# Kernel optimization log

Hardware: AMD Instinct MI355X
Metric: run time of the kernel (lower is better)

Reference implementation:

```python
import jax, jax.numpy as jnp
from jax import lax
import numpy as np

IN_DIM = 5
HID = 512
SEQ = 250
BATCH = 256


def setup_inputs() -> dict:
    key = jax.random.key(0)
    ks = jax.random.split(key, 7)
    s = 1.0 / np.sqrt(HID)  # PyTorch LSTMCell init scale
    strokes = jax.random.normal(ks[0], (BATCH, SEQ, IN_DIM), dtype=jnp.float32)
    W_ih = jax.random.uniform(ks[1], (4 * HID, IN_DIM), minval=-s, maxval=s, dtype=jnp.float32)
    W_hh = jax.random.uniform(ks[2], (4 * HID, HID), minval=-s, maxval=s, dtype=jnp.float32)
    b_ih = jax.random.uniform(ks[3], (4 * HID,), minval=-s, maxval=s, dtype=jnp.float32)
    b_hh = jax.random.uniform(ks[4], (4 * HID,), minval=-s, maxval=s, dtype=jnp.float32)
    W_out = jax.random.uniform(ks[5], (1, HID), minval=-s, maxval=s, dtype=jnp.float32)
    b_out = jax.random.uniform(ks[6], (1,), minval=-s, maxval=s, dtype=jnp.float32)
    return {"strokes": strokes, "W_ih": W_ih, "W_hh": W_hh, "b_ih": b_ih,
            "b_hh": b_hh, "W_out": W_out, "b_out": b_out}


def reference(strokes, W_ih, W_hh, b_ih, b_hh, W_out, b_out):
    B = strokes.shape[0]
    # Precompute input projections for all timesteps (one big GEMM instead of SEQ small ones)
    # x_proj: [T, B, 4H]
    x_proj = jnp.einsum('bti,gi->tbg', strokes, W_ih) + b_ih + b_hh
    h0 = jnp.zeros((B, HID), dtype=strokes.dtype)
    c0 = jnp.zeros((B, HID), dtype=strokes.dtype)

    def step(carry, xp):
        h, c = carry
        gates = xp + h @ W_hh.T  # [B, 4H]; PyTorch gate order: i, f, g, o
        i, f, g, o = jnp.split(gates, 4, axis=-1)
        c = jax.nn.sigmoid(f) * c + jax.nn.sigmoid(i) * jnp.tanh(g)
        h = jax.nn.sigmoid(o) * jnp.tanh(c)
        return (h, c), None

    (h, _), _ = lax.scan(step, (h0, c0), x_proj)
    raw = (h @ W_out.T + b_out).squeeze(-1)  # [B]
    return jax.nn.sigmoid(jax.nn.leaky_relu(raw, 0.1))
```

## Files before the change

kernel.cpp:

```cpp
#include <hip/hip_runtime.h>
#include <hip/hip_bf16.h>

#define BATCH 256
#define SEQ   250
#define HID   512
#define INDIM 5

#define NBLK  256
#define NCH   16
#define MB    16
#define HB    32
#define NMEM  16

#define LROWU 36
#define LMEMU 576
#define SLOT_BYTES (BATCH * HID * 2)

typedef __attribute__((ext_vector_type(8))) short short8;
typedef __attribute__((ext_vector_type(4))) float f32x4;
typedef __attribute__((ext_vector_type(4))) unsigned int u32x4;

__device__ __forceinline__ float sigmoidf_fast(float x) {
  return 1.0f / (1.0f + __expf(-x));
}
__device__ __forceinline__ float tanhf_fast(float x) {
  return 2.0f / (1.0f + __expf(-2.0f * x)) - 1.0f;
}
__device__ __forceinline__ unsigned short f2bf_rne(float x) {
  union { float f; unsigned u; } v; v.f = x;
  unsigned r = v.u + 0x7fffu + ((v.u >> 16) & 1u);
  return (unsigned short)(r >> 16);
}
__device__ __forceinline__ float bf2f(unsigned short h) {
  union { unsigned u; float f; } v; v.u = ((unsigned)h) << 16;
  return v.f;
}

__global__ __launch_bounds__(256, 1) void lstm_persist(
    const float* __restrict__ strokes, const float* __restrict__ W_ih,
    const float* __restrict__ W_hh, const float* __restrict__ b_ih,
    const float* __restrict__ b_hh, const float* __restrict__ W_out,
    const float* __restrict__ b_out, float* __restrict__ out,
    unsigned short* __restrict__ hbuf,
    int* __restrict__ flagsML,
    int* __restrict__ flagsL2,
    int* __restrict__ xcd_ids,
    int* __restrict__ vflag)
{
  const int tid  = threadIdx.x;
  const int bid  = blockIdx.x;
  const int bt   = bid & 15;
  const int ht   = bid >> 4;
  const int wv   = tid >> 6;
  const int lane = tid & 63;
  const int n16  = lane & 15;
  const int q    = lane >> 4;

  __shared__ unsigned short h_lds[NMEM * LMEMU];
  __shared__ float g_lds[4][MB][33];
  __shared__ float wih_lds[4][HB][INDIM];
  __shared__ float bias_lds[4][HB];
  __shared__ int fast_s;

  unsigned xcc;
  asm volatile("s_getreg_b32 %0, hwreg(HW_REG_XCC_ID)" : "=s"(xcc));
  xcc &= 0xfu;
  if (tid == 0) {
    __hip_atomic_store(&xcd_ids[bid], (int)xcc, __ATOMIC_RELAXED,
                       __HIP_MEMORY_SCOPE_AGENT);
  }
  if (bid < 16 && wv == 0) {
    int other = (int)xcc;
    if (lane < NMEM) {
      const int* xp = &xcd_ids[bid + 16 * lane];
      other = -1;
      for (int it = 0; it < 16384 && other < 0; ++it) {
        other = __hip_atomic_load(xp, __ATOMIC_RELAXED, __HIP_MEMORY_SCOPE_AGENT);
      }
    }
    unsigned long long ok = __ballot(other == (int)xcc);
    if (lane == 0) {
      __hip_atomic_store(&vflag[bid * 16], (ok == ~0ull) ? 2 : 1,
                         __ATOMIC_RELAXED, __HIP_MEMORY_SCOPE_AGENT);
    }
  }
  if (tid == 0) {
    int v;
    do {
      v = __hip_atomic_load(&vflag[bt * 16], __ATOMIC_RELAXED,
                            __HIP_MEMORY_SCOPE_AGENT);
    } while (v <= 0);
    fast_s = (v == 2) ? 1 : 0;
  }

  if (tid < 128) {
    int g = tid >> 5, j = tid & 31;
    int r = g * HID + ht * HB + j;
    #pragma unroll
    for (int i = 0; i < INDIM; ++i) wih_lds[g][j][i] = W_ih[r * INDIM + i];
    bias_lds[g][j] = b_ih[r] + b_hh[r];
  }

  short8 wfrag[16][2];
  {
    #pragma unroll
    for (int i = 0; i < 16; ++i) {
      const int kb = (wv * 4 + i) & 15;
      #pragma unroll
      for (int nt = 0; nt < 2; ++nt) {
        const float* p = W_hh
            + (size_t)(wv * HID + ht * HB + nt * 16 + n16) * HID
            + kb * 32 + q * 8;
        short8 f;
        #pragma unroll
        for (int j = 0; j < 8; ++j) f[j] = (short)f2bf_rne(p[j]);
        wfrag[i][nt] = f;
      }
    }
  }
  __syncthreads();
  const bool fast = fast_s != 0;

  const int am  = tid >> 4;
  const int ajp = (tid & 15) * 2;
  const int ab  = bt * MB + am;
  const int j0m = wv * 4;
  float c0 = 0.f, c1 = 0.f;

  for (int t = 0; t < SEQ; ++t) {
    unsigned short* hprev = hbuf + (((t & 1) ^ 1) ? (SLOT_BYTES / 2) : 0);
    unsigned short* hcur  = hbuf + ((t & 1) ? (SLOT_BYTES / 2) : 0);

    const float* sp = strokes + ((size_t)ab * SEQ + t) * INDIM;
    float s0 = sp[0], s1 = sp[1], s2 = sp[2], s3 = sp[3], s4 = sp[4];

    f32x4 acc[2][2] = {};
    if (t > 0) {
      if (lane < 16) {
        const int fi = (bt * 16 + (j0m + (lane >> 2))) * 16 + (lane & 3) * 4;
        const int* fpL = &flagsL2[fi];
        const int* fpM = &flagsML[fi];
        if (fast) {
          int v;
          do {
            int v1, v2;
            asm volatile("global_load_dword %0, %2, off sc0\n\t"
                         "global_load_dword %1, %3, off sc0 sc1\n\t"
                         "s_waitcnt vmcnt(0)"
                         : "=v"(v1), "=v"(v2)
                         : "v"(fpL), "v"(fpM)
                         : "memory");
            v = v1 > v2 ? v1 : v2;
          } while (v < t);
        } else {
          while (__hip_atomic_load(fpM, __ATOMIC_RELAXED,
                                   __HIP_MEMORY_SCOPE_AGENT) < t) { }
        }
      }
      const char* base = reinterpret_cast<const char*>(hprev) + bt * 16384
                       + j0m * 1024;
      u32x4 tmp[4];
      if (fast) {
        #pragma unroll
        for (int i = 0; i < 4; ++i)
          asm volatile("global_load_dwordx4 %0, %1, off sc0"
                       : "=v"(tmp[i])
                       : "v"(base + (size_t)(i * 64 + lane) * 16) : "memory");
      } else {
        #pragma unroll
        for (int i = 0; i < 4; ++i)
          asm volatile("global_load_dwordx4 %0, %1, off sc0 sc1"
                       : "=v"(tmp[i])
                       : "v"(base + (size_t)(i * 64 + lane) * 16) : "memory");
      }
      asm volatile("s_waitcnt vmcnt(0)" ::: "memory");
      #pragma unroll
      for (int i = 0; i < 4; ++i) {
        const int idx = i * 64 + lane;
        const int m   = j0m + (idx >> 6);
        const int c   = idx & 63;
        *reinterpret_cast<u32x4*>(
            &h_lds[m * LMEMU + (c >> 2) * LROWU + (c & 3) * 8]) = tmp[i];
      }

      #pragma unroll
      for (int i = 0; i < 4; ++i) {
        const int kb = wv * 4 + i;
        const short8 a = *reinterpret_cast<const short8*>(
            &h_lds[kb * LMEMU + n16 * LROWU + q * 8]);
        #pragma unroll
        for (int nt = 0; nt < 2; ++nt)
          acc[nt][i & 1] = __builtin_amdgcn_mfma_f32_16x16x32_bf16(
              a, wfrag[i][nt], acc[nt][i & 1], 0, 0, 0);
      }
      __syncthreads();
      #pragma unroll
      for (int i = 4; i < 16; ++i) {
        const int kb = (wv * 4 + i) & 15;
        const short8 a = *reinterpret_cast<const short8*>(
            &h_lds[kb * LMEMU + n16 * LROWU + q * 8]);
        #pragma unroll
        for (int nt = 0; nt < 2; ++nt)
          acc[nt][i & 1] = __builtin_amdgcn_mfma_f32_16x16x32_bf16(
              a, wfrag[i][nt], acc[nt][i & 1], 0, 0, 0);
      }
    }

    #pragma unroll
    for (int nt = 0; nt < 2; ++nt) {
      #pragma unroll
      for (int r = 0; r < 4; ++r) {
        g_lds[wv][q * 4 + r][nt * 16 + n16] = acc[nt][0][r] + acc[nt][1][r];
      }
    }
    __syncthreads();

    float hv[2];
    #pragma unroll
    for (int e = 0; e < 2; ++e) {
      const int j = ajp + e;
      float pre[4];
      #pragma unroll
      for (int g = 0; g < 4; ++g) {
        pre[g] = bias_lds[g][j] + g_lds[g][am][j]
               + s0 * wih_lds[g][j][0] + s1 * wih_lds[g][j][1]
               + s2 * wih_lds[g][j][2] + s3 * wih_lds[g][j][3]
               + s4 * wih_lds[g][j][4];
      }
      float ig = sigmoidf_fast(pre[0]);
      float fg = sigmoidf_fast(pre[1]);
      float gg = tanhf_fast(pre[2]);
      float og = sigmoidf_fast(pre[3]);
      float& c = e ? c1 : c0;
      c = fg * c + ig * gg;
      hv[e] = og * tanhf_fast(c);
    }
    unsigned pack = (unsigned)f2bf_rne(hv[0]) | ((unsigned)f2bf_rne(hv[1]) << 16);
    unsigned* hp = reinterpret_cast<unsigned*>(
        reinterpret_cast<char*>(hcur) + bt * 16384 + ht * 1024 + am * 64 + ajp * 2);
    if (fast) {
      asm volatile("global_store_dword %0, %1, off sc0"
                   :: "v"(hp), "v"(pack) : "memory");
    } else {
      __hip_atomic_store(hp, pack, __ATOMIC_RELAXED, __HIP_MEMORY_SCOPE_AGENT);
    }

    asm volatile("s_waitcnt vmcnt(0)" ::: "memory");
    const int gen = t + 1;
    if (lane == 0) {
      const int fi = (bt * 16 + ht) * 16 + wv * 4;
      if (fast) {
        asm volatile("global_store_dword %0, %1, off sc0"
                     :: "v"(&flagsL2[fi]), "v"(gen) : "memory");
      }
      __hip_atomic_store(&flagsML[fi], gen, __ATOMIC_RELAXED,
                         __HIP_MEMORY_SCOPE_AGENT);
    }
  }

  if (ht == 0) {
    if (lane < 16) {
      const int fi = (bt * 16 + (j0m + (lane >> 2))) * 16 + (lane & 3) * 4;
      const int* fpL = &flagsL2[fi];
      const int* fpM = &flagsML[fi];
      if (fast) {
        int v;
        do {
          int v1, v2;
          asm volatile("global_load_dword %0, %2, off sc0\n\t"
                       "global_load_dword %1, %3, off sc0 sc1\n\t"
                       "s_waitcnt vmcnt(0)"
                       : "=v"(v1), "=v"(v2)
                       : "v"(fpL), "v"(fpM)
                       : "memory");
          v = v1 > v2 ? v1 : v2;
        } while (v < SEQ);
      } else {
        while (__hip_atomic_load(fpM, __ATOMIC_RELAXED,
                                 __HIP_MEMORY_SCOPE_AGENT) < SEQ) { }
      }
    }
    const char* base = reinterpret_cast<const char*>(hbuf)
                     + ((SEQ - 1) & 1) * SLOT_BYTES + bt * 16384 + j0m * 1024;
    u32x4 tmp[4];
    if (fast) {
      #pragma unroll
      for (int i = 0; i < 4; ++i)
        asm volatile("global_load_dwordx4 %0, %1, off sc0"
                     : "=v"(tmp[i])
                     : "v"(base + (size_t)(i * 64 + lane) * 16) : "memory");
    } else {
      #pragma unroll
      for (int i = 0; i < 4; ++i)
        asm volatile("global_load_dwordx4 %0, %1, off sc0 sc1"
                     : "=v"(tmp[i])
                     : "v"(base + (size_t)(i * 64 + lane) * 16) : "memory");
    }
    asm volatile("s_waitcnt vmcnt(0)" ::: "memory");
    #pragma unroll
    for (int i = 0; i < 4; ++i) {
      const int idx = i * 64 + lane;
      const int m   = j0m + (idx >> 6);
      const int c   = idx & 63;
      *reinterpret_cast<u32x4*>(
          &h_lds[m * LMEMU + (c >> 2) * LROWU + (c & 3) * 8]) = tmp[i];
    }
    __syncthreads();
    if (tid < MB) {
      const int b = bt * MB + tid;
      float s = 0.f;
      for (int k = 0; k < HID; ++k) {
        s += bf2f(h_lds[(k >> 5) * LMEMU + tid * LROWU + (k & 31)]) * W_out[k];
      }
      float raw = s + b_out[0];
      float lr = raw > 0.f ? raw : 0.1f * raw;
      out[b] = 1.0f / (1.0f + __expf(-lr));
    }
  }
}

extern "C" void kernel_launch(void* const* d_in, const int* in_sizes, int n_in,
                              void* d_out, int out_size, void* d_ws, size_t ws_size,
                              hipStream_t stream) {
  const float* strokes = (const float*)d_in[0];
  const float* W_ih    = (const float*)d_in[1];
  const float* W_hh    = (const float*)d_in[2];
  const float* b_ih    = (const float*)d_in[3];
  const float* b_hh    = (const float*)d_in[4];
  const float* W_out   = (const float*)d_in[5];
  const float* b_out   = (const float*)d_in[6];
  float* out = (float*)d_out;

  char* ws = (char*)d_ws;
  unsigned short* hbuf = (unsigned short*)ws;
  size_t off = (size_t)2 * SLOT_BYTES;
  int* flagsML = (int*)(ws + off);  off += 16384;
  int* flagsL2 = (int*)(ws + off);  off += 16384;
  int* xcd_ids = (int*)(ws + off);  off += 2048;
  int* vflag   = (int*)(ws + off);

  lstm_persist<<<NBLK, 256, 0, stream>>>(strokes, W_ih, W_hh, b_ih, b_hh,
                                         W_out, b_out, out, hbuf,
                                         flagsML, flagsL2, xcd_ids, vflag);
}
```

Measured before the change: 849.1 us.

## Halve block count and interleave two independent batch chains per block

Each block now handles two batch chains (16-row groups) for its hidden slice, alternating between them each timestep, with 128 blocks instead of 256. The aim is to hide the cross-block flag-wait latency of one chain behind the compute of the other, and to halve the total number of participating blocks. The trade-off is half as many CUs running, roughly twice the serial work per block per step, and extra barriers in the t=0 path.

After: 1.073 ms. 1.26x slower.

```diff
diff --git a/kernel.cpp b/kernel.cpp
--- a/kernel.cpp
+++ b/kernel.cpp
@@ -6,7 +6,7 @@
 #define HID   512
 #define INDIM 5
 
-#define NBLK  256
+#define NBLK  128
 #define NCH   16
 #define MB    16
 #define HB    32
@@ -49,8 +49,8 @@
 {
   const int tid  = threadIdx.x;
   const int bid  = blockIdx.x;
-  const int bt   = bid & 15;
-  const int ht   = bid >> 4;
+  const int p    = bid & 7;
+  const int m    = bid >> 3;
   const int wv   = tid >> 6;
   const int lane = tid & 63;
   const int n16  = lane & 15;
@@ -69,10 +69,10 @@
     __hip_atomic_store(&xcd_ids[bid], (int)xcc, __ATOMIC_RELAXED,
                        __HIP_MEMORY_SCOPE_AGENT);
   }
-  if (bid < 16 && wv == 0) {
+  if (bid < 8 && wv == 0) {
     int other = (int)xcc;
     if (lane < NMEM) {
-      const int* xp = &xcd_ids[bid + 16 * lane];
+      const int* xp = &xcd_ids[lane * 8 + p];
       other = -1;
       for (int it = 0; it < 16384 && other < 0; ++it) {
         other = __hip_atomic_load(xp, __ATOMIC_RELAXED, __HIP_MEMORY_SCOPE_AGENT);
@@ -80,14 +80,14 @@
     }
     unsigned long long ok = __ballot(other == (int)xcc);
     if (lane == 0) {
-      __hip_atomic_store(&vflag[bid * 16], (ok == ~0ull) ? 2 : 1,
+      __hip_atomic_store(&vflag[p * 16], (ok == ~0ull) ? 2 : 1,
                          __ATOMIC_RELAXED, __HIP_MEMORY_SCOPE_AGENT);
     }
   }
   if (tid == 0) {
     int v;
     do {
-      v = __hip_atomic_load(&vflag[bt * 16], __ATOMIC_RELAXED,
+      v = __hip_atomic_load(&vflag[p * 16], __ATOMIC_RELAXED,
                             __HIP_MEMORY_SCOPE_AGENT);
     } while (v <= 0);
     fast_s = (v == 2) ? 1 : 0;
@@ -95,7 +95,7 @@
 
   if (tid < 128) {
     int g = tid >> 5, j = tid & 31;
-    int r = g * HID + ht * HB + j;
+    int r = g * HID + m * HB + j;
     #pragma unroll
     for (int i = 0; i < INDIM; ++i) wih_lds[g][j][i] = W_ih[r * INDIM + i];
     bias_lds[g][j] = b_ih[r] + b_hh[r];
@@ -108,12 +108,12 @@
       const int kb = (wv * 4 + i) & 15;
       #pragma unroll
       for (int nt = 0; nt < 2; ++nt) {
-        const float* p = W_hh
-            + (size_t)(wv * HID + ht * HB + nt * 16 + n16) * HID
+        const float* pw = W_hh
+            + (size_t)(wv * HID + m * HB + nt * 16 + n16) * HID
             + kb * 32 + q * 8;
         short8 f;
         #pragma unroll
-        for (int j = 0; j < 8; ++j) f[j] = (short)f2bf_rne(p[j]);
+        for (int j = 0; j < 8; ++j) f[j] = (short)f2bf_rne(pw[j]);
         wfrag[i][nt] = f;
       }
     }
@@ -123,13 +123,16 @@
 
   const int am  = tid >> 4;
   const int ajp = (tid & 15) * 2;
-  const int ab  = bt * MB + am;
   const int j0m = wv * 4;
-  float c0 = 0.f, c1 = 0.f;
-
-  for (int t = 0; t < SEQ; ++t) {
-    unsigned short* hprev = hbuf + (((t & 1) ^ 1) ? (SLOT_BYTES / 2) : 0);
-    unsigned short* hcur  = hbuf + ((t & 1) ? (SLOT_BYTES / 2) : 0);
+  float cst[2][2] = {{0.f, 0.f}, {0.f, 0.f}};
+
+  auto phase = [&](int ci, int t) {
+    const int chain = p * 2 + ci;
+    const int ab    = chain * MB + am;
+    char* hslotprev = reinterpret_cast<char*>(hbuf)
+                    + (((t & 1) ^ 1) ? SLOT_BYTES : 0);
+    char* hslotcur  = reinterpret_cast<char*>(hbuf)
+                    + ((t & 1) ? SLOT_BYTES : 0);
 
     const float* sp = strokes + ((size_t)ab * SEQ + t) * INDIM;
     float s0 = sp[0], s1 = sp[1], s2 = sp[2], s3 = sp[3], s4 = sp[4];
@@ -137,7 +140,7 @@
     f32x4 acc[2][2] = {};
     if (t > 0) {
       if (lane < 16) {
-        const int fi = (bt * 16 + (j0m + (lane >> 2))) * 16 + (lane & 3) * 4;
+        const int fi = (chain * 16 + (j0m + (lane >> 2))) * 16 + (lane & 3) * 4;
         const int* fpL = &flagsL2[fi];
         const int* fpM = &flagsML[fi];
         if (fast) {
@@ -157,8 +160,7 @@
                                    __HIP_MEMORY_SCOPE_AGENT) < t) { }
         }
       }
-      const char* base = reinterpret_cast<const char*>(hprev) + bt * 16384
-                       + j0m * 1024;
+      const char* base = hslotprev + chain * 16384 + j0m * 1024;
       u32x4 tmp[4];
       if (fast) {
         #pragma unroll
@@ -177,10 +179,10 @@
       #pragma unroll
       for (int i = 0; i < 4; ++i) {
         const int idx = i * 64 + lane;
-        const int m   = j0m + (idx >> 6);
+        const int mm  = j0m + (idx >> 6);
         const int c   = idx & 63;
         *reinterpret_cast<u32x4*>(
-            &h_lds[m * LMEMU + (c >> 2) * LROWU + (c & 3) * 8]) = tmp[i];
+            &h_lds[mm * LMEMU + (c >> 2) * LROWU + (c & 3) * 8]) = tmp[i];
       }
 
       #pragma unroll
@@ -204,6 +206,8 @@
           acc[nt][i & 1] = __builtin_amdgcn_mfma_f32_16x16x32_bf16(
               a, wfrag[i][nt], acc[nt][i & 1], 0, 0, 0);
       }
+    } else {
+      __syncthreads();
     }
 
     #pragma unroll
@@ -231,13 +235,13 @@
       float fg = sigmoidf_fast(pre[1]);
       float gg = tanhf_fast(pre[2]);
       float og = sigmoidf_fast(pre[3]);
-      float& c = e ? c1 : c0;
+      float& c = cst[ci][e];
       c = fg * c + ig * gg;
       hv[e] = og * tanhf_fast(c);
     }
     unsigned pack = (unsigned)f2bf_rne(hv[0]) | ((unsigned)f2bf_rne(hv[1]) << 16);
     unsigned* hp = reinterpret_cast<unsigned*>(
-        reinterpret_cast<char*>(hcur) + bt * 16384 + ht * 1024 + am * 64 + ajp * 2);
+        hslotcur + chain * 16384 + m * 1024 + am * 64 + ajp * 2);
     if (fast) {
       asm volatile("global_store_dword %0, %1, off sc0"
                    :: "v"(hp), "v"(pack) : "memory");
@@ -248,7 +252,7 @@
     asm volatile("s_waitcnt vmcnt(0)" ::: "memory");
     const int gen = t + 1;
     if (lane == 0) {
-      const int fi = (bt * 16 + ht) * 16 + wv * 4;
+      const int fi = (chain * 16 + m) * 16 + wv * 4;
       if (fast) {
         asm volatile("global_store_dword %0, %1, off sc0"
                      :: "v"(&flagsL2[fi]), "v"(gen) : "memory");
@@ -256,65 +260,76 @@
       __hip_atomic_store(&flagsML[fi], gen, __ATOMIC_RELAXED,
                          __HIP_MEMORY_SCOPE_AGENT);
     }
-  }
-
-  if (ht == 0) {
-    if (lane < 16) {
-      const int fi = (bt * 16 + (j0m + (lane >> 2))) * 16 + (lane & 3) * 4;
-      const int* fpL = &flagsL2[fi];
-      const int* fpM = &flagsML[fi];
+  };
+
+  for (int t = 0; t < SEQ; ++t) {
+    phase(0, t);
+    phase(1, t);
+  }
+
+  if (m == 0) {
+    #pragma unroll 1
+    for (int ci = 0; ci < 2; ++ci) {
+      const int chain = p * 2 + ci;
+      if (lane < 16) {
+        const int fi = (chain * 16 + (j0m + (lane >> 2))) * 16 + (lane & 3) * 4;
+        const int* fpL = &flagsL2[fi];
+        const int* fpM = &flagsML[fi];
+        if (fast) {
+          int v;
+          do {
+            int v1, v2;
+            asm volatile("global_load_dword %0, %2, off sc0\n\t"
+                         "global_load_dword %1, %3, off sc0 sc1\n\t"
+                         "s_waitcnt vmcnt(0)"
+                         : "=v"(v1), "=v"(v2)
+                         : "v"(fpL), "v"(fpM)
+                         : "memory");
+            v = v1 > v2 ? v1 : v2;
+          } while (v < SEQ);
+        } else {
+          while (__hip_atomic_load(fpM, __ATOMIC_RELAXED,
+                                   __HIP_MEMORY_SCOPE_AGENT) < SEQ) { }
+        }
+      }
+      const char* base = reinterpret_cast<const char*>(hbuf)
+                       + ((SEQ - 1) & 1) * SLOT_BYTES + chain * 16384
+                       + j0m * 1024;
+      u32x4 tmp[4];
       if (fast) {
-        int v;
-        do {
-          int v1, v2;
-          asm volatile("global_load_dword %0, %2, off sc0\n\t"
-                       "global_load_dword %1, %3, off sc0 sc1\n\t"
-                       "s_waitcnt vmcnt(0)"
-                       : "=v"(v1), "=v"(v2)
-                       : "v"(fpL), "v"(fpM)
-                       : "memory");
-          v = v1 > v2 ? v1 : v2;
-        } while (v < SEQ);
+        #pragma unroll
+        for (int i = 0; i < 4; ++i)
+          asm volatile("global_load_dwordx4 %0, %1, off sc0"
+                       : "=v"(tmp[i])
+                       : "v"(base + (size_t)(i * 64 + lane) * 16) : "memory");
       } else {
-        while (__hip_atomic_load(fpM, __ATOMIC_RELAXED,
-                                 __HIP_MEMORY_SCOPE_AGENT) < SEQ) { }
-      }
-    }
-    const char* base = reinterpret_cast<const char*>(hbuf)
-                     + ((SEQ - 1) & 1) * SLOT_BYTES + bt * 16384 + j0m * 1024;
-    u32x4 tmp[4];
-    if (fast) {
-      #pragma unroll
-      for (int i = 0; i < 4; ++i)
-        asm volatile("global_load_dwordx4 %0, %1, off sc0"
-                     : "=v"(tmp[i])
-                     : "v"(base + (size_t)(i * 64 + lane) * 16) : "memory");
-    } else {
-      #pragma unroll
-      for (int i = 0; i < 4; ++i)
-        asm volatile("global_load_dwordx4 %0, %1, off sc0 sc1"
-                     : "=v"(tmp[i])
-                     : "v"(base + (size_t)(i * 64 + lane) * 16) : "memory");
-    }
-    asm volatile("s_waitcnt vmcnt(0)" ::: "memory");
-    #pragma unroll
-    for (int i = 0; i < 4; ++i) {
-      const int idx = i * 64 + lane;
-      const int m   = j0m + (idx >> 6);
-      const int c   = idx & 63;
-      *reinterpret_cast<u32x4*>(
-          &h_lds[m * LMEMU + (c >> 2) * LROWU + (c & 3) * 8]) = tmp[i];
-    }
-    __syncthreads();
-    if (tid < MB) {
-      const int b = bt * MB + tid;
-      float s = 0.f;
-      for (int k = 0; k < HID; ++k) {
-        s += bf2f(h_lds[(k >> 5) * LMEMU + tid * LROWU + (k & 31)]) * W_out[k];
-      }
-      float raw = s + b_out[0];
-      float lr = raw > 0.f ? raw : 0.1f * raw;
-      out[b] = 1.0f / (1.0f + __expf(-lr));
+        #pragma unroll
+        for (int i = 0; i < 4; ++i)
+          asm volatile("global_load_dwordx4 %0, %1, off sc0 sc1"
+                       : "=v"(tmp[i])
+                       : "v"(base + (size_t)(i * 64 + lane) * 16) : "memory");
+      }
+      asm volatile("s_waitcnt vmcnt(0)" ::: "memory");
+      #pragma unroll
+      for (int i = 0; i < 4; ++i) {
+        const int idx = i * 64 + lane;
+        const int mm  = j0m + (idx >> 6);
+        const int c   = idx & 63;
+        *reinterpret_cast<u32x4*>(
+            &h_lds[mm * LMEMU + (c >> 2) * LROWU + (c & 3) * 8]) = tmp[i];
+      }
+      __syncthreads();
+      if (tid < MB) {
+        const int b = chain * MB + tid;
+        float s = 0.f;
+        for (int k = 0; k < HID; ++k) {
+          s += bf2f(h_lds[(k >> 5) * LMEMU + tid * LROWU + (k & 31)]) * W_out[k];
+        }
+        float raw = s + b_out[0];
+        float lr = raw > 0.f ? raw : 0.1f * raw;
+        out[b] = 1.0f / (1.0f + __expf(-lr));
+      }
+      __syncthreads();
     }
   }
 }
```

## Load full h tile per wave directly into MFMA registers, skip LDS staging

Applied to the files above, without the earlier changes.

Each wave now polls all 64 producer flags itself and loads the full 16x512 bf16 h tile straight from global memory into A-fragment registers. This removes the cooperative LDS staging, the LDS writes and reads, and the mid-step __syncthreads. In exchange, each wave issues four times more global loads (16 dwordx4 instead of 4) and waits on all producers before starting any MFMA, so it loses the overlap of the first four k-blocks with the other producers.

New measurement: 976.2 us. 15.0% more time.

```diff
diff --git a/kernel.cpp b/kernel.cpp
--- a/kernel.cpp
+++ b/kernel.cpp
@@ -12,8 +12,6 @@
 #define HB    32
 #define NMEM  16
 
-#define LROWU 36
-#define LMEMU 576
 #define SLOT_BYTES (BATCH * HID * 2)
 
 typedef __attribute__((ext_vector_type(8))) short short8;
@@ -35,6 +33,14 @@
   union { unsigned u; float f; } v; v.u = ((unsigned)h) << 16;
   return v.f;
 }
+
+#define AF_DRAIN(af) \
+  asm volatile("s_waitcnt vmcnt(0)" \
+               : "+v"(af[0]), "+v"(af[1]), "+v"(af[2]), "+v"(af[3]), \
+                 "+v"(af[4]), "+v"(af[5]), "+v"(af[6]), "+v"(af[7]), \
+                 "+v"(af[8]), "+v"(af[9]), "+v"(af[10]), "+v"(af[11]), \
+                 "+v"(af[12]), "+v"(af[13]), "+v"(af[14]), "+v"(af[15]) \
+               :: "memory")
 
 __global__ __launch_bounds__(256, 1) void lstm_persist(
     const float* __restrict__ strokes, const float* __restrict__ W_ih,
@@ -56,10 +62,10 @@
   const int n16  = lane & 15;
   const int q    = lane >> 4;
 
-  __shared__ unsigned short h_lds[NMEM * LMEMU];
   __shared__ float g_lds[4][MB][33];
   __shared__ float wih_lds[4][HB][INDIM];
   __shared__ float bias_lds[4][HB];
+  __shared__ unsigned short h_fin[NMEM * 576];
   __shared__ int fast_s;
 
   unsigned xcc;
@@ -104,8 +110,7 @@
   short8 wfrag[16][2];
   {
     #pragma unroll
-    for (int i = 0; i < 16; ++i) {
-      const int kb = (wv * 4 + i) & 15;
+    for (int kb = 0; kb < 16; ++kb) {
       #pragma unroll
       for (int nt = 0; nt < 2; ++nt) {
         const float* p = W_hh
@@ -114,7 +119,7 @@
         short8 f;
         #pragma unroll
         for (int j = 0; j < 8; ++j) f[j] = (short)f2bf_rne(p[j]);
-        wfrag[i][nt] = f;
+        wfrag[kb][nt] = f;
       }
     }
   }
@@ -124,22 +129,24 @@
   const int am  = tid >> 4;
   const int ajp = (tid & 15) * 2;
   const int ab  = bt * MB + am;
-  const int j0m = wv * 4;
+  const int pfi = (bt * 16 + (lane >> 2)) * 16 + (lane & 3) * 4;
+  const int aoff = n16 * 64 + q * 16;
   float c0 = 0.f, c1 = 0.f;
 
   for (int t = 0; t < SEQ; ++t) {
-    unsigned short* hprev = hbuf + (((t & 1) ^ 1) ? (SLOT_BYTES / 2) : 0);
-    unsigned short* hcur  = hbuf + ((t & 1) ? (SLOT_BYTES / 2) : 0);
+    char* hslotprev = reinterpret_cast<char*>(hbuf)
+                    + (((t & 1) ^ 1) ? SLOT_BYTES : 0);
+    char* hslotcur  = reinterpret_cast<char*>(hbuf)
+                    + ((t & 1) ? SLOT_BYTES : 0);
 
     const float* sp = strokes + ((size_t)ab * SEQ + t) * INDIM;
     float s0 = sp[0], s1 = sp[1], s2 = sp[2], s3 = sp[3], s4 = sp[4];
 
     f32x4 acc[2][2] = {};
     if (t > 0) {
-      if (lane < 16) {
-        const int fi = (bt * 16 + (j0m + (lane >> 2))) * 16 + (lane & 3) * 4;
-        const int* fpL = &flagsL2[fi];
-        const int* fpM = &flagsML[fi];
+      {
+        const int* fpL = &flagsL2[pfi];
+        const int* fpM = &flagsML[pfi];
         if (fast) {
           int v;
           do {
@@ -157,52 +164,27 @@
                                    __HIP_MEMORY_SCOPE_AGENT) < t) { }
         }
       }
-      const char* base = reinterpret_cast<const char*>(hprev) + bt * 16384
-                       + j0m * 1024;
-      u32x4 tmp[4];
+      const char* base = hslotprev + bt * 16384 + aoff;
+      u32x4 af[16];
       if (fast) {
         #pragma unroll
-        for (int i = 0; i < 4; ++i)
+        for (int kb = 0; kb < 16; ++kb)
           asm volatile("global_load_dwordx4 %0, %1, off sc0"
-                       : "=v"(tmp[i])
-                       : "v"(base + (size_t)(i * 64 + lane) * 16) : "memory");
+                       : "=v"(af[kb]) : "v"(base + kb * 1024) : "memory");
       } else {
         #pragma unroll
-        for (int i = 0; i < 4; ++i)
+        for (int kb = 0; kb < 16; ++kb)
           asm volatile("global_load_dwordx4 %0, %1, off sc0 sc1"
-                       : "=v"(tmp[i])
-                       : "v"(base + (size_t)(i * 64 + lane) * 16) : "memory");
-      }
-      asm volatile("s_waitcnt vmcnt(0)" ::: "memory");
-      #pragma unroll
-      for (int i = 0; i < 4; ++i) {
-        const int idx = i * 64 + lane;
-        const int m   = j0m + (idx >> 6);
-        const int c   = idx & 63;
-        *reinterpret_cast<u32x4*>(
-            &h_lds[m * LMEMU + (c >> 2) * LROWU + (c & 3) * 8]) = tmp[i];
-      }
-
-      #pragma unroll
-      for (int i = 0; i < 4; ++i) {
-        const int kb = wv * 4 + i;
-        const short8 a = *reinterpret_cast<const short8*>(
-            &h_lds[kb * LMEMU + n16 * LROWU + q * 8]);
+                       : "=v"(af[kb]) : "v"(base + kb * 1024) : "memory");
+      }
+      AF_DRAIN(af);
+      #pragma unroll
+      for (int kb = 0; kb < 16; ++kb) {
+        const short8 a = *reinterpret_cast<const short8*>(&af[kb]);
         #pragma unroll
         for (int nt = 0; nt < 2; ++nt)
-          acc[nt][i & 1] = __builtin_amdgcn_mfma_f32_16x16x32_bf16(
-              a, wfrag[i][nt], acc[nt][i & 1], 0, 0, 0);
-      }
-      __syncthreads();
-      #pragma unroll
-      for (int i = 4; i < 16; ++i) {
-        const int kb = (wv * 4 + i) & 15;
-        const short8 a = *reinterpret_cast<const short8*>(
-            &h_lds[kb * LMEMU + n16 * LROWU + q * 8]);
-        #pragma unroll
-        for (int nt = 0; nt < 2; ++nt)
-          acc[nt][i & 1] = __builtin_amdgcn_mfma_f32_16x16x32_bf16(
-              a, wfrag[i][nt], acc[nt][i & 1], 0, 0, 0);
+          acc[nt][kb & 1] = __builtin_amdgcn_mfma_f32_16x16x32_bf16(
+              a, wfrag[kb][nt], acc[nt][kb & 1], 0, 0, 0);
       }
     }
 
@@ -237,7 +219,7 @@
     }
     unsigned pack = (unsigned)f2bf_rne(hv[0]) | ((unsigned)f2bf_rne(hv[1]) << 16);
     unsigned* hp = reinterpret_cast<unsigned*>(
-        reinterpret_cast<char*>(hcur) + bt * 16384 + ht * 1024 + am * 64 + ajp * 2);
+        hslotcur + bt * 16384 + ht * 1024 + am * 64 + ajp * 2);
     if (fast) {
       asm volatile("global_store_dword %0, %1, off sc0"
                    :: "v"(hp), "v"(pack) : "memory");
@@ -259,10 +241,9 @@
   }
 
   if (ht == 0) {
-    if (lane < 16) {
-      const int fi = (bt * 16 + (j0m + (lane >> 2))) * 16 + (lane & 3) * 4;
-      const int* fpL = &flagsL2[fi];
-      const int* fpM = &flagsML[fi];
+    {
+      const int* fpL = &flagsL2[pfi];
+      const int* fpM = &flagsML[pfi];
       if (fast) {
         int v;
         do {
@@ -281,7 +262,8 @@
       }
     }
     const char* base = reinterpret_cast<const char*>(hbuf)
-                     + ((SEQ - 1) & 1) * SLOT_BYTES + bt * 16384 + j0m * 1024;
+                     + ((SEQ - 1) & 1) * SLOT_BYTES + bt * 16384
+                     + (wv * 4) * 1024;
     u32x4 tmp[4];
     if (fast) {
       #pragma unroll
@@ -300,17 +282,17 @@
     #pragma unroll
     for (int i = 0; i < 4; ++i) {
       const int idx = i * 64 + lane;
-      const int m   = j0m + (idx >> 6);
+      const int mm  = wv * 4 + (idx >> 6);
       const int c   = idx & 63;
       *reinterpret_cast<u32x4*>(
-          &h_lds[m * LMEMU + (c >> 2) * LROWU + (c & 3) * 8]) = tmp[i];
+          &h_fin[mm * 576 + (c >> 2) * 36 + (c & 3) * 8]) = tmp[i];
     }
     __syncthreads();
     if (tid < MB) {
       const int b = bt * MB + tid;
       float s = 0.f;
       for (int k = 0; k < HID; ++k) {
-        s += bf2f(h_lds[(k >> 5) * LMEMU + tid * LROWU + (k & 31)]) * W_out[k];
+        s += bf2f(h_fin[(k >> 5) * 576 + tid * 36 + (k & 31)]) * W_out[k];
       }
       float raw = s + b_out[0];
       float lr = raw > 0.f ? raw : 0.1f * raw;
```
